# Optimization experiments

Hardware: AMD Instinct MI355X
Metric: run time of the kernel (lower is better)

The kernel has to match this reference:

```python
import jax, jax.numpy as jnp
import numpy as np

B, S, D, HEADS, E, HID = 4, 2048, 512, 8, 8, 1365  # HID = int(D*4*2/3) per Expert_alt
CF, THRESH, TOPN = 2.0, 0.2, 2                      # capacity_factor_eval, threshold_eval, top-2
BAL_COEF, Z_COEF = 0.01, 0.001


def setup_inputs():
    key = jax.random.key(0)
    ks = jax.random.split(key, 8)
    f32 = jnp.float32
    return {
        'x': jax.random.normal(ks[0], (B, S, D), f32),
        'Wqkv': jax.random.normal(ks[1], (3 * D, D), f32) * (D ** -0.5),
        'bqkv': jnp.zeros((3 * D,), f32),
        'Wo': jax.random.normal(ks[2], (D, D), f32) * (D ** -0.5),
        'bo': jnp.zeros((D,), f32),
        'Wg': jax.random.normal(ks[3], (D, E), f32) * (D ** -0.5),
        'ln_g': jnp.ones((E, D), f32),
        'ln_b': jnp.zeros((E, D), f32),
        'W1': jax.random.normal(ks[4], (E, D, HID), f32) * (D ** -0.5),
        'b1': jnp.zeros((E, HID), f32),
        'W2': jax.random.normal(ks[5], (E, HID, D), f32) * (HID ** -0.5),
        'b2': jnp.zeros((E, D), f32),
    }


def _moe(x, Wg, ln_g, ln_b, W1, b1, W2, b2):
    # top-2 gated MoE with capacity-factor dispatch, grouped expert FFN, combine
    Bq, Sq, Dq = x.shape
    Eq = Wg.shape[1]
    C = int(CF * Sq * TOPN / Eq)  # expert capacity per batch row
    logits = x @ Wg                              # [B,S,E]
    probs = jax.nn.softmax(logits, -1)
    gvals, gidx = jax.lax.top_k(probs, 2)        # [B,S,2]
    use2 = (gvals[..., 1] > THRESH).astype(x.dtype)
    # priority order: all top-1 assignments first, then top-2
    e_idx = jnp.concatenate([gidx[..., 0], gidx[..., 1]], axis=1)          # [B,2S]
    assigned = jnp.concatenate([jnp.ones((Bq, Sq), x.dtype), use2], axis=1)
    onehot = jax.nn.one_hot(e_idx, Eq, dtype=x.dtype) * assigned[..., None]
    pos = (jnp.cumsum(onehot, axis=1) * onehot).sum(-1) - 1.0              # slot within expert
    keep = ((assigned > 0) & (pos >= 0) & (pos < C)).astype(x.dtype)
    slot = jnp.where(keep > 0, pos, C).astype(jnp.int32)                   # overflow -> slot C (dropped)
    b_idx = jnp.broadcast_to(jnp.arange(Bq)[:, None], (Bq, 2 * Sq))
    x2 = jnp.concatenate([x, x], axis=1) * keep[..., None]
    disp = jnp.zeros((Bq, Eq, C + 1, Dq), x.dtype).at[b_idx, e_idx, slot].add(x2)
    # grouped expert FFN: LayerNorm -> Linear -> LeakyReLU -> Linear
    xe = disp[:, :, :C].transpose(1, 0, 2, 3).reshape(Eq, Bq * C, Dq)
    mu = xe.mean(-1, keepdims=True)
    var = xe.var(-1, keepdims=True)
    xn = (xe - mu) * jax.lax.rsqrt(var + 1e-5) * ln_g[:, None] + ln_b[:, None]
    h = jnp.einsum('etd,edh->eth', xn, W1) + b1[:, None]
    h = jnp.where(h > 0, h, 0.01 * h)  # LeakyReLU
    ye = jnp.einsum('eth,ehd->etd', h, W2) + b2[:, None]
    yb = ye.reshape(Eq, Bq, C, Dq).transpose(1, 0, 2, 3)                   # [B,E,C,D]
    yb = jnp.concatenate([yb, jnp.zeros((Bq, Eq, 1, Dq), x.dtype)], axis=2)
    y_tok = yb[b_idx, e_idx, slot]                                         # [B,2S,D]
    w = jnp.concatenate([gvals[..., 0], gvals[..., 1] * use2], axis=1) * keep
    out = (y_tok * w[..., None]).reshape(Bq, 2, Sq, Dq).sum(1)
    # aux losses
    top1 = jax.nn.one_hot(gidx[..., 0], Eq, dtype=x.dtype)
    density = top1.mean((0, 1))
    proxy = probs.mean((0, 1))
    balance = Eq * jnp.sum(density * proxy)
    zloss = jnp.mean(jax.nn.logsumexp(logits, -1) ** 2)
    total = BAL_COEF * balance + Z_COEF * zloss
    return out, total, balance, zloss


def reference(x, Wqkv, bqkv, Wo, bo, Wg, ln_g, ln_b, W1, b1, W2, b2):
    Bq, Sq, Dq = x.shape
    dh = Dq // HEADS
    qkv = x @ Wqkv.T + bqkv
    q, k, v = jnp.split(qkv, 3, -1)
    rs = lambda t: t.reshape(Bq, Sq, HEADS, dh).transpose(0, 2, 1, 3)
    q, k, v = rs(q), rs(k), rs(v)
    attn = jax.nn.softmax(jnp.einsum('bhqd,bhkd->bhqk', q, k) / np.float32(np.sqrt(dh)), -1)
    o = jnp.einsum('bhqk,bhkd->bhqd', attn, v).transpose(0, 2, 1, 3).reshape(Bq, Sq, Dq)
    o = o @ Wo.T + bo + x  # MHA + residual
    moe_out, total, bal, z = _moe(o, Wg, ln_g, ln_b, W1, b1, W2, b2)
    return moe_out + o, total, bal, z  # SparseMoEBlock residual; dropout is identity (eval)
```

## Files before the change

kernel.cpp:

```cpp
#include <hip/hip_runtime.h>
#include <hip/hip_bf16.h>
#include <math.h>

#define B_    4
#define S_    2048
#define D_    512
#define H_    8
#define DH_   64
#define E_    8
#define HID_  1365
#define HIDP_ 1408
#define CAP_  1024
#define TOK_  (B_*S_)
#define NASS_ (B_*2*S_)
#define RMAX_ (NASS_ + 8*128)
#define NQKU_ 1152
#define C11   (1.0f/2048.0f)
#define C22   (1.0f/(2048.0f*2048.0f))

typedef __attribute__((ext_vector_type(8))) short bf16x8;
typedef __attribute__((ext_vector_type(8))) _Float16 f16x8;
typedef __attribute__((ext_vector_type(4))) float f32x4;
typedef __hip_bfloat16 bf16;
typedef _Float16 f16;

#define MFMA16(a, b, c) __builtin_amdgcn_mfma_f32_16x16x32_bf16(a, b, c, 0, 0, 0)
#define MFMAH(a, b, c)  __builtin_amdgcn_mfma_f32_16x16x32_f16(a, b, c, 0, 0, 0)

__device__ __forceinline__ void gload16(const void* g, void* l) {
  __builtin_amdgcn_global_load_lds(
      (const __attribute__((address_space(1))) unsigned int*)g,
      (__attribute__((address_space(3))) unsigned int*)l, 16, 0, 0);
}

__device__ __forceinline__ unsigned bf16pk(float a, float b) {
  unsigned ua = __float_as_uint(a); ua = (ua + 0x7FFF + ((ua >> 16) & 1)) >> 16;
  unsigned ub = __float_as_uint(b); ub = (ub + 0x7FFF + ((ub >> 16) & 1)) >> 16;
  return ua | (ub << 16);
}

__device__ __forceinline__ unsigned short h2us(f16 h) {
  return *(unsigned short*)&h;
}

__global__ __launch_bounds__(256) void cvt_bf16(const float* __restrict__ in,
                                                bf16* __restrict__ out, int n) {
  int i = (blockIdx.x * 256 + threadIdx.x) * 4;
  if (i < n) {
    float4 v = *(const float4*)(in + i);
    uint2 pk; pk.x = bf16pk(v.x, v.y); pk.y = bf16pk(v.z, v.w);
    *(uint2*)((unsigned short*)out + i) = pk;
  }
}

__global__ __launch_bounds__(256) void cvt_f16(const float* __restrict__ in,
                                               f16* __restrict__ out, int n) {
  int i = (blockIdx.x * 256 + threadIdx.x) * 4;
  if (i < n) {
    float4 v = *(const float4*)(in + i);
    ushort4 o;
    ((unsigned short*)&o)[0] = h2us((f16)v.x);
    ((unsigned short*)&o)[1] = h2us((f16)v.y);
    ((unsigned short*)&o)[2] = h2us((f16)v.z);
    ((unsigned short*)&o)[3] = h2us((f16)v.w);
    *(ushort4*)((unsigned short*)out + i) = o;
  }
}

__global__ __launch_bounds__(256) void split2h(const float* __restrict__ in,
    unsigned short* __restrict__ ph, unsigned short* __restrict__ pl, int n) {
  int i = (blockIdx.x * 256 + threadIdx.x) * 4;
  if (i >= n) return;
  float4 v = *(const float4*)(in + i);
  float a[4] = {v.x, v.y, v.z, v.w};
  ushort4 hh, ll;
#pragma unroll
  for (int j = 0; j < 4; j++) {
    f16 h = (f16)a[j];
    float r = (a[j] - (float)h) * 2048.f;
    f16 l = (f16)r;
    ((unsigned short*)&hh)[j] = h2us(h);
    ((unsigned short*)&ll)[j] = h2us(l);
  }
  *(ushort4*)(ph + i) = hh;
  *(ushort4*)(pl + i) = ll;
}

__global__ __launch_bounds__(256) void transpose_w1(const float* __restrict__ W1,
                                                    bf16* __restrict__ W1t) {
  __shared__ float t[32][33];
  int e = blockIdx.z;
  int n0 = blockIdx.x * 32, d0 = blockIdx.y * 32;
  int tx = threadIdx.x & 31, ty = threadIdx.x >> 5;
  const float* in = W1 + (size_t)e * D_ * HID_;
  bf16* out = W1t + (size_t)e * HIDP_ * D_;
#pragma unroll
  for (int j = 0; j < 4; j++) {
    int d = d0 + ty + j * 8, n = n0 + tx;
    t[ty + j * 8][tx] = (n < HID_) ? in[(size_t)d * HID_ + n] : 0.f;
  }
  __syncthreads();
#pragma unroll
  for (int j = 0; j < 4; j++) {
    int n = n0 + ty + j * 8, d = d0 + tx;
    out[(size_t)n * D_ + d] = __float2bfloat16(t[tx][ty + j * 8]);
  }
}

__global__ __launch_bounds__(256) void transpose_w2(const float* __restrict__ W2,
                                                    bf16* __restrict__ W2t) {
  __shared__ float t[32][33];
  int e = blockIdx.z;
  int n0 = blockIdx.x * 32, k0 = blockIdx.y * 32;
  int tx = threadIdx.x & 31, ty = threadIdx.x >> 5;
  const float* in = W2 + (size_t)e * HID_ * D_;
  bf16* out = W2t + (size_t)e * D_ * HIDP_;
#pragma unroll
  for (int j = 0; j < 4; j++) {
    int k = k0 + ty + j * 8;
    t[ty + j * 8][tx] = (k < HID_) ? in[(size_t)k * D_ + n0 + tx] : 0.f;
  }
  __syncthreads();
#pragma unroll
  for (int j = 0; j < 4; j++) {
    int n = n0 + ty + j * 8, k = k0 + tx;
    out[(size_t)n * HIDP_ + k] = __float2bfloat16(t[tx][ty + j * 8]);
  }
}

__global__ __launch_bounds__(256) void transpose_v(const unsigned short* __restrict__ vbuf,
                                                   unsigned short* __restrict__ vT) {
  __shared__ unsigned short t[32][33];
  int bh = blockIdx.z;
  int b = bh >> 3, h = bh & 7;
  int s0 = blockIdx.x * 32, d0 = blockIdx.y * 32;
  int tx = threadIdx.x & 31, ty = threadIdx.x >> 5;
  const unsigned short* in = vbuf + (size_t)b * S_ * D_ + h * DH_;
#pragma unroll
  for (int j = 0; j < 4; j++)
    t[ty + j * 8][tx] = in[(size_t)(s0 + ty + j * 8) * D_ + d0 + tx];
  __syncthreads();
  unsigned short* out = vT + (size_t)bh * DH_ * S_;
#pragma unroll
  for (int j = 0; j < 4; j++)
    out[(size_t)(d0 + ty + j * 8) * S_ + s0 + tx] = t[tx][ty + j * 8];
}

__global__ __launch_bounds__(256) void transpose_u(const float* __restrict__ qku,
                                                   f16* __restrict__ U2T) {
  __shared__ float t[64][132];
  int b = blockIdx.y;
  int s0 = blockIdx.x * 64;
  int tid = threadIdx.x;
#pragma unroll
  for (int p = 0; p < 8; p++) {
    int i = tid + p * 256;
    int tok = i >> 5, c4 = i & 31;
    float4 v = *(const float4*)(qku + (size_t)(b * 2048 + s0 + tok) * NQKU_ + 1024 + c4 * 4);
    t[tok][c4 * 4 + 0] = v.x; t[tok][c4 * 4 + 1] = v.y;
    t[tok][c4 * 4 + 2] = v.z; t[tok][c4 * 4 + 3] = v.w;
  }
  __syncthreads();
  int row = tid >> 1, sh = tid & 1;
  int h = row >> 4, rr = row & 15;
  int e = rr & 7;
  bool lo = rr >= 8;
  f16* dst = U2T + ((size_t)((b * 8 + h) * 16 + rr) * 2048 + s0 + sh * 32);
  for (int i = 0; i < 32; i++) {
    float v = t[sh * 32 + i][h * 8 + e];
    f16 hh = (f16)v;
    f16 outv = lo ? (f16)((v - (float)hh) * 2048.f) : hh;
    dst[i] = outv;
  }
}

template <int MODE>
__global__ __launch_bounds__(256) void gemm_mfma(
    const bf16* __restrict__ A, const bf16* __restrict__ Bt,
    const float* __restrict__ bias, const float* __restrict__ resid,
    void* __restrict__ Cout, int N, int K,
    const int* __restrict__ ebase, const int* __restrict__ ecnt) {
  __shared__ bf16 Al[128 * 64];
  __shared__ bf16 Bl[128 * 64];
  int tid = threadIdx.x;
  int w = tid >> 6, lane = tid & 63;
  int lg = lane >> 4, li = lane & 15;
  int e = 0;
  size_t arow0;
  if constexpr (MODE >= 2) {
    e = blockIdx.z;
    int r0 = blockIdx.y * 128;
    if (r0 >= ecnt[e]) return;
    arow0 = (size_t)(ebase[e] + r0);
  } else {
    arow0 = (size_t)blockIdx.y * 128;
  }
  int n0 = blockIdx.x * 128;
  const bf16* Bexp = Bt + (size_t)e * N * K;

  int rowA[4], scA[4];
#pragma unroll
  for (int j = 0; j < 4; j++) {
    int o = w * 4096 + j * 1024 + lane * 16;
    rowA[j] = o >> 7;
    scA[j] = ((o >> 4) & 7) ^ (rowA[j] & 7);
  }
  int wm = w >> 1, wn = w & 1;
  f32x4 acc[4][4] = {};

  for (int k0 = 0; k0 < K; k0 += 64) {
#pragma unroll
    for (int j = 0; j < 4; j++) {
      int o = w * 4096 + j * 1024 + lane * 16;
      gload16(A + (arow0 + rowA[j]) * (size_t)K + k0 + scA[j] * 8, (char*)Al + o);
      gload16(Bexp + (size_t)(n0 + rowA[j]) * K + k0 + scA[j] * 8, (char*)Bl + o);
    }
    __syncthreads();
#pragma unroll
    for (int ks = 0; ks < 2; ks++) {
      bf16x8 af[4], bfr[4];
#pragma unroll
      for (int mi = 0; mi < 4; mi++) {
        int row = wm * 64 + mi * 16 + li;
        int cb = (lg * 16 + ks * 64) ^ ((row & 7) << 4);
        af[mi] = *(const bf16x8*)((char*)Al + row * 128 + cb);
      }
#pragma unroll
      for (int ni = 0; ni < 4; ni++) {
        int row = wn * 64 + ni * 16 + li;
        int cb = (lg * 16 + ks * 64) ^ ((row & 7) << 4);
        bfr[ni] = *(const bf16x8*)((char*)Bl + row * 128 + cb);
      }
#pragma unroll
      for (int mi = 0; mi < 4; mi++)
#pragma unroll
        for (int ni = 0; ni < 4; ni++)
          acc[mi][ni] = MFMA16(af[mi], bfr[ni], acc[mi][ni]);
    }
    __syncthreads();
  }

#pragma unroll
  for (int mi = 0; mi < 4; mi++) {
#pragma unroll
    for (int ni = 0; ni < 4; ni++) {
#pragma unroll
      for (int r = 0; r < 4; r++) {
        size_t m = arow0 + wm * 64 + mi * 16 + lg * 4 + r;
        int c = n0 + wn * 64 + ni * 16 + li;
        float v = acc[mi][ni][r];
        if constexpr (MODE == 1) {
          v += bias[c] + resid[m * (size_t)N + c];
          ((float*)Cout)[m * (size_t)N + c] = v;
        } else if constexpr (MODE == 2) {
          if (c < HID_) {
            v += bias[e * HID_ + c];
            v = (v > 0.f) ? v : 0.01f * v;
            ((bf16*)Cout)[m * (size_t)HIDP_ + c] = __float2bfloat16(v);
          } else {
            ((bf16*)Cout)[m * (size_t)HIDP_ + c] = __float2bfloat16(0.f);
          }
        } else {
          v += bias[e * D_ + c];
          ((bf16*)Cout)[m * (size_t)N + c] = __float2bfloat16(v);
        }
      }
    }
  }
}

__global__ __launch_bounds__(256) void gemm_vf16(
    const f16* __restrict__ A, const f16* __restrict__ Bt,
    const float* __restrict__ bias, f16* __restrict__ Cout, int N, int K) {
  __shared__ f16 Al[128 * 64];
  __shared__ f16 Bl[128 * 64];
  int tid = threadIdx.x;
  int w = tid >> 6, lane = tid & 63;
  int lg = lane >> 4, li = lane & 15;
  size_t arow0 = (size_t)blockIdx.y * 128;
  int n0 = blockIdx.x * 128;

  int rowA[4], scA[4];
#pragma unroll
  for (int j = 0; j < 4; j++) {
    int o = w * 4096 + j * 1024 + lane * 16;
    rowA[j] = o >> 7;
    scA[j] = ((o >> 4) & 7) ^ (rowA[j] & 7);
  }
  int wm = w >> 1, wn = w & 1;
  f32x4 acc[4][4] = {};

  for (int k0 = 0; k0 < K; k0 += 64) {
#pragma unroll
    for (int j = 0; j < 4; j++) {
      int o = w * 4096 + j * 1024 + lane * 16;
      gload16(A + (arow0 + rowA[j]) * (size_t)K + k0 + scA[j] * 8, (char*)Al + o);
      gload16(Bt + (size_t)(n0 + rowA[j]) * K + k0 + scA[j] * 8, (char*)Bl + o);
    }
    __syncthreads();
#pragma unroll
    for (int ks = 0; ks < 2; ks++) {
      f16x8 af[4], bfr[4];
#pragma unroll
      for (int mi = 0; mi < 4; mi++) {
        int row = wm * 64 + mi * 16 + li;
        int cb = (lg * 16 + ks * 64) ^ ((row & 7) << 4);
        af[mi] = *(const f16x8*)((char*)Al + row * 128 + cb);
      }
#pragma unroll
      for (int ni = 0; ni < 4; ni++) {
        int row = wn * 64 + ni * 16 + li;
        int cb = (lg * 16 + ks * 64) ^ ((row & 7) << 4);
        bfr[ni] = *(const f16x8*)((char*)Bl + row * 128 + cb);
      }
#pragma unroll
      for (int mi = 0; mi < 4; mi++)
#pragma unroll
        for (int ni = 0; ni < 4; ni++)
          acc[mi][ni] = MFMAH(af[mi], bfr[ni], acc[mi][ni]);
    }
    __syncthreads();
  }
#pragma unroll
  for (int mi = 0; mi < 4; mi++)
#pragma unroll
    for (int ni = 0; ni < 4; ni++)
#pragma unroll
      for (int r = 0; r < 4; r++) {
        size_t m = arow0 + wm * 64 + mi * 16 + lg * 4 + r;
        int c = n0 + wn * 64 + ni * 16 + li;
        Cout[m * (size_t)N + c] = (f16)(acc[mi][ni][r] + bias[c]);
      }
}

__global__ __launch_bounds__(256) void gemm_split2(
    const f16* __restrict__ Ah, const f16* __restrict__ Als,
    const f16* __restrict__ Bh, const f16* __restrict__ Bls,
    const float* __restrict__ bias, float* __restrict__ C, int N, int K) {
  __shared__ f16 Ls[4][128 * 32];
  const f16* Ap[2] = {Ah, Als};
  const f16* Bp[2] = {Bh, Bls};
  int tid = threadIdx.x;
  int w = tid >> 6, lane = tid & 63;
  int lg = lane >> 4, li = lane & 15;
  int lin = blockIdx.y * gridDim.x + blockIdx.x;
  int aa = lin / 72, t = lin % 72;
  size_t m0 = (size_t)((t & 7) + 8 * aa) * 128;
  int n0 = (t >> 3) * 128;
  int wm = w >> 1, wn = w & 1;
  f32x4 accA[4][4] = {};
  f32x4 accB[4][4] = {};

  for (int k0 = 0; k0 < K; k0 += 32) {
#pragma unroll
    for (int p = 0; p < 2; p++) {
#pragma unroll
      for (int j = 0; j < 2; j++) {
        int o = w * 2048 + j * 1024 + lane * 16;
        int row = o >> 6;
        int sc = ((o >> 4) & 3) ^ (row & 3);
        gload16(Ap[p] + (m0 + row) * (size_t)K + k0 + sc * 8, (char*)Ls[p] + o);
        gload16(Bp[p] + (size_t)(n0 + row) * K + k0 + sc * 8, (char*)Ls[2 + p] + o);
      }
    }
    __syncthreads();
    f16x8 afh[4], afl[4], bfh[4], bfl[4];
#pragma unroll
    for (int mi = 0; mi < 4; mi++) {
      int row = wm * 64 + mi * 16 + li;
      int cb = (lg * 16) ^ ((row & 3) << 4);
      afh[mi] = *(const f16x8*)((char*)Ls[0] + row * 64 + cb);
      afl[mi] = *(const f16x8*)((char*)Ls[1] + row * 64 + cb);
    }
#pragma unroll
    for (int ni = 0; ni < 4; ni++) {
      int row = wn * 64 + ni * 16 + li;
      int cb = (lg * 16) ^ ((row & 3) << 4);
      bfh[ni] = *(const f16x8*)((char*)Ls[2] + row * 64 + cb);
      bfl[ni] = *(const f16x8*)((char*)Ls[3] + row * 64 + cb);
    }
#pragma unroll
    for (int mi = 0; mi < 4; mi++)
#pragma unroll
      for (int ni = 0; ni < 4; ni++) {
        accA[mi][ni] = MFMAH(afh[mi], bfh[ni], accA[mi][ni]);
        accB[mi][ni] = MFMAH(afh[mi], bfl[ni], accB[mi][ni]);
        accB[mi][ni] = MFMAH(afl[mi], bfh[ni], accB[mi][ni]);
      }
    __syncthreads();
  }
#pragma unroll
  for (int mi = 0; mi < 4; mi++)
#pragma unroll
    for (int ni = 0; ni < 4; ni++)
#pragma unroll
      for (int r = 0; r < 4; r++) {
        size_t m = m0 + wm * 64 + mi * 16 + lg * 4 + r;
        int c = n0 + wn * 64 + ni * 16 + li;
        C[m * (size_t)N + c] = accA[mi][ni][r] + accB[mi][ni][r] * C11 + bias[c];
      }
}

__global__ __launch_bounds__(256) void ksplit(const float* __restrict__ qku,
    unsigned short* __restrict__ kh, unsigned short* __restrict__ kls) {
  int gid = blockIdx.x * 256 + threadIdx.x;
  int idx4 = gid * 4;
  int t = idx4 >> 9, c = idx4 & 511;
  int h = c >> 6, d = c & 63;
  int b = t >> 11, s = t & 2047;
  float4 v = *(const float4*)(qku + (size_t)t * NQKU_ + 512 + c);
  float a[4] = {v.x, v.y, v.z, v.w};
  ushort4 hh, ll;
#pragma unroll
  for (int j = 0; j < 4; j++) {
    f16 hv = (f16)a[j];
    f16 lv = (f16)((a[j] - (float)hv) * 2048.f);
    ((unsigned short*)&hh)[j] = h2us(hv);
    ((unsigned short*)&ll)[j] = h2us(lv);
  }
  size_t o = (((size_t)(b * 8 + h) * S_ + s) * 64 + d);
  *(ushort4*)(kh + o) = hh;
  *(ushort4*)(kls + o) = ll;
}

__global__ __launch_bounds__(256) void wg2_kernel(const float* __restrict__ Wo,
                                                  const float* __restrict__ Wg,
                                                  float* __restrict__ Wg2) {
  int gid = blockIdx.x * 256 + threadIdx.x;
  int d = gid >> 3, e = gid & 7;
  float acc = 0.f;
  for (int n = 0; n < D_; n++) acc += Wo[(size_t)n * D_ + d] * Wg[n * E_ + e];
  Wg2[d * E_ + e] = acc;
}

__global__ __launch_bounds__(256) void wu_kernel(const float* __restrict__ Wqkv,
    const float* __restrict__ Wg2, const float* __restrict__ bqkv,
    float* __restrict__ Wu, float* __restrict__ bfull) {
  int gid = blockIdx.x * 256 + threadIdx.x;
  int row = gid >> 9, d = gid & 511;
  float acc = 0.f;
  if (row < 64) {
    int h = row >> 3, e = row & 7;
    const float* wv = Wqkv + (size_t)(1024 + h * 64) * 512 + d;
    const float* wg = Wg2 + h * 64 * 8 + e;
    for (int c = 0; c < 64; c++) acc += wv[(size_t)c * 512] * wg[c * 8];
  }
  Wu[gid] = acc;
  if (gid < 1024) bfull[gid] = bqkv[gid];
  if (gid < 128) {
    float bacc = 0.f;
    if (gid < 64) {
      int h = gid >> 3, e = gid & 7;
      for (int c = 0; c < 64; c++)
        bacc += bqkv[1024 + h * 64 + c] * Wg2[(h * 64 + c) * 8 + e];
    }
    bfull[1024 + gid] = bacc;
  }
}

__global__ __launch_bounds__(256) void xwg_kernel(const float* __restrict__ x,
                                                  const float* __restrict__ bo,
                                                  const float* __restrict__ Wg,
                                                  float* __restrict__ logits) {
  int tid = threadIdx.x;
  int tl = tid >> 3, j = tid & 7;
  int t = blockIdx.x * 32 + tl;
  const float* xr = x + (size_t)t * D_;
  float part[8] = {0, 0, 0, 0, 0, 0, 0, 0};
  for (int d = j; d < D_; d += 8) {
    float xv = xr[d] + bo[d];
    const float* wg = Wg + d * E_;
#pragma unroll
    for (int e = 0; e < 8; e++) part[e] += xv * wg[e];
  }
#pragma unroll
  for (int off = 1; off < 8; off <<= 1)
#pragma unroll
    for (int e = 0; e < 8; e++) part[e] += __shfl_xor(part[e], off);
  if (j == 0) {
#pragma unroll
    for (int e = 0; e < 8; e++) logits[(size_t)t * 8 + e] = part[e];
  }
}

__global__ __launch_bounds__(512, 4) void attn_fused(
    const float* __restrict__ qku,
    const f16* __restrict__ kh, const f16* __restrict__ kls,
    const f16* __restrict__ vT, const f16* __restrict__ U2T,
    bf16* __restrict__ attnb, float* __restrict__ part) {
  __shared__ f16 Ks0[128 * 64];
  __shared__ f16 Ks1[128 * 64];
  __shared__ f16 Vtl[64 * 128];
  __shared__ f16 Ut[16 * 128];
  __shared__ f16 Pl[8][16 * 40];
  int bid = blockIdx.x;
  int xcd = bid & 7, idx = bid >> 3;
  int bh = (idx >> 4) * 8 + xcd;
  int qt = idx & 15;
  int b = bh >> 3, h = bh & 7, q0 = qt * 128;
  int tid = threadIdx.x, w = tid >> 6, lane = tid & 63;
  int lg = lane >> 4, qi = lane & 15;

  const float* qsrc = qku + (size_t)(b * S_ + q0 + w * 16 + qi) * NQKU_ + h * 64 + lg * 8;
  f16x8 qh[2], qls[2];
#pragma unroll
  for (int ks = 0; ks < 2; ks++) {
#pragma unroll
    for (int i = 0; i < 8; i++) {
      float xv = qsrc[ks * 32 + i];
      f16 hh = (f16)xv;
      f16 ll = (f16)((xv - (float)hh) * 2048.f);
      qh[ks][i] = hh;
      qls[ks][i] = ll;
    }
  }

  f32x4 oacc[4] = {};
  f32x4 raccA = {0.f, 0.f, 0.f, 0.f};
  f32x4 raccB = {0.f, 0.f, 0.f, 0.f};
  float mrun = -1e30f, lrun = 0.f;
  const f16* Vbase = vT + (size_t)bh * DH_ * S_;
  char* pw = (char*)&Pl[w][0];

  for (int kt = 0; kt < S_ / 128; kt++) {
#pragma unroll
    for (int j = 0; j < 2; j++) {
      int o = w * 2048 + j * 1024 + lane * 16;
      int row = o >> 7;
      int sc = ((o >> 4) & 7) ^ (row & 7);
      size_t srcK = ((size_t)bh * S_ + kt * 128 + row) * 64 + sc * 8;
      gload16(kh + srcK, (char*)Ks0 + o);
      gload16(kls + srcK, (char*)Ks1 + o);
      int rowv = o >> 8;
      int scv = ((o >> 4) & 15) ^ (rowv & 7);
      gload16(Vbase + (size_t)rowv * S_ + kt * 128 + scv * 8, (char*)Vtl + o);
    }
    if (w < 2) {
#pragma unroll
      for (int j = 0; j < 2; j++) {
        int o = w * 2048 + j * 1024 + lane * 16;
        int rowu = o >> 8;
        int scu = ((o >> 4) & 15) ^ (rowu & 7);
        gload16(U2T + ((size_t)(bh * 16 + rowu) * 2048 + kt * 128 + scu * 8),
                (char*)Ut + o);
      }
    }
    __syncthreads();

    f32x4 sA[8], sB[8];
#pragma unroll
    for (int nb = 0; nb < 8; nb++) {
      f32x4 z = {0.f, 0.f, 0.f, 0.f};
      sA[nb] = z; sB[nb] = z;
    }
#pragma unroll
    for (int ks = 0; ks < 2; ks++) {
#pragma unroll
      for (int nb = 0; nb < 8; nb++) {
        int row = nb * 16 + qi;
        int cb = (lg * 16 + ks * 64) ^ ((row & 7) << 4);
        f16x8 k0 = *(const f16x8*)((char*)Ks0 + row * 128 + cb);
        f16x8 k1 = *(const f16x8*)((char*)Ks1 + row * 128 + cb);
        sA[nb] = MFMAH(k0, qh[ks], sA[nb]);
        sB[nb] = MFMAH(k0, qls[ks], sB[nb]);
        sB[nb] = MFMAH(k1, qh[ks], sB[nb]);
      }
    }
    float tmax = -1e30f;
#pragma unroll
    for (int nb = 0; nb < 8; nb++)
#pragma unroll
      for (int r = 0; r < 4; r++) {
        float v = (sA[nb][r] + sB[nb][r] * C11) * 0.125f;
        sA[nb][r] = v;
        tmax = fmaxf(tmax, v);
      }
    tmax = fmaxf(tmax, __shfl_xor(tmax, 16));
    tmax = fmaxf(tmax, __shfl_xor(tmax, 32));
    float mnew = fmaxf(mrun, tmax);
    float fsc = __expf(mrun - mnew);
    float psum = 0.f;
#pragma unroll
    for (int nb = 0; nb < 8; nb++)
#pragma unroll
      for (int r = 0; r < 4; r++) {
        float pv = __expf(sA[nb][r] - mnew);
        sA[nb][r] = pv;
        psum += pv;
      }
    psum += __shfl_xor(psum, 16);
    psum += __shfl_xor(psum, 32);
    lrun = lrun * fsc + psum;
    mrun = mnew;
#pragma unroll
    for (int r = 0; r < 4; r++) { raccA[r] *= fsc; raccB[r] *= fsc; }
#pragma unroll
    for (int db = 0; db < 4; db++)
#pragma unroll
      for (int r = 0; r < 4; r++) oacc[db][r] *= fsc;

#pragma unroll
    for (int c = 0; c < 4; c++) {
      float pv[8]; f16 phv[8];
#pragma unroll
      for (int nbL = 0; nbL < 2; nbL++)
#pragma unroll
        for (int rp = 0; rp < 2; rp++) {
          int nb = c * 2 + nbL;
          float p0 = sA[nb][rp * 2], p1 = sA[nb][rp * 2 + 1];
          f16 h0 = (f16)p0, h1 = (f16)p1;
          int ii = (nbL * 2 + rp) * 2;
          pv[ii] = p0; pv[ii + 1] = p1; phv[ii] = h0; phv[ii + 1] = h1;
          unsigned wd = (unsigned)h2us(h0) | ((unsigned)h2us(h1) << 16);
          int keyl = 4 * lg + 2 * rp + 16 * nbL;
          *(unsigned*)(pw + qi * 80 + keyl * 2) = wd;
        }
      f16x8 pf = *(const f16x8*)(pw + qi * 80 + lg * 16);
#pragma unroll
      for (int db = 0; db < 4; db++) {
        int row = db * 16 + qi;
        int cb = (lg * 16 + c * 64) ^ ((row & 7) << 4);
        f16x8 vf = *(const f16x8*)((char*)Vtl + row * 256 + cb);
        oacc[db] = MFMAH(vf, pf, oacc[db]);
      }
      int ua = qi * 256 + ((c * 64 + lg * 16) ^ ((qi & 7) << 4));
      f16x8 uf = *(const f16x8*)((char*)Ut + ua);
      raccA = MFMAH(uf, pf, raccA);
#pragma unroll
      for (int nbL = 0; nbL < 2; nbL++)
#pragma unroll
        for (int rp = 0; rp < 2; rp++) {
          int ii = (nbL * 2 + rp) * 2;
          f16 l0 = (f16)((pv[ii] - (float)phv[ii]) * 2048.f);
          f16 l1 = (f16)((pv[ii + 1] - (float)phv[ii + 1]) * 2048.f);
          unsigned wd = (unsigned)h2us(l0) | ((unsigned)h2us(l1) << 16);
          int keyl = 4 * lg + 2 * rp + 16 * nbL;
          *(unsigned*)(pw + qi * 80 + keyl * 2) = wd;
        }
      f16x8 pfl = *(const f16x8*)(pw + qi * 80 + lg * 16);
      raccB = MFMAH(uf, pfl, raccB);
    }
    __syncthreads();
  }

  float inv = 1.f / lrun;
  f32x4 pA, pB;
#pragma unroll
  for (int r = 0; r < 4; r++) {
    pA[r] = __shfl_xor(raccA[r], 32);
    pB[r] = __shfl_xor(raccB[r], 32);
  }
  if (lg < 2) {
    float* dst = part + ((size_t)bh * S_ + q0 + w * 16 + qi) * 8 + lg * 4;
#pragma unroll
    for (int r = 0; r < 4; r++)
      dst[r] = (raccA[r] + C11 * (pA[r] + raccB[r]) + C22 * pB[r]) * inv;
  }
  char* ow = (char*)Ks0 + w * 2048;
#pragma unroll
  for (int db = 0; db < 4; db++)
#pragma unroll
    for (int rp = 0; rp < 2; rp++) {
      int d = db * 16 + lg * 4 + rp * 2;
      unsigned pk = bf16pk(oacc[db][rp * 2] * inv, oacc[db][rp * 2 + 1] * inv);
      int addr = (qi * 128 + d * 2) ^ ((qi & 7) << 4);
      *(unsigned*)(ow + addr) = pk;
    }
#pragma unroll
  for (int j = 0; j < 2; j++) {
    int o = j * 1024 + lane * 16;
    int q = o >> 7;
    int c16 = (o >> 4) & 7;
    int sc = c16 ^ (q & 7);
    bf16x8 vv = *(const bf16x8*)(ow + q * 128 + sc * 16);
    *(bf16x8*)(attnb + ((size_t)(b * S_ + q0 + w * 16 + q)) * D_ + h * DH_ + c16 * 8) = vv;
  }
}

__global__ __launch_bounds__(256) void reduce_gate(
    const float* __restrict__ xwg, const float* __restrict__ part,
    int* __restrict__ e1a, int* __restrict__ e2a,
    float* __restrict__ g1a, float* __restrict__ g2a, int* __restrict__ use2a,
    float* __restrict__ dacc) {
  int t = blockIdx.x * 256 + threadIdx.x;
  int b = t >> 11, s = t & 2047;
  float lg[8];
#pragma unroll
  for (int e = 0; e < 8; e++) lg[e] = xwg[(size_t)t * 8 + e];
  for (int h = 0; h < 8; h++) {
    const float* pp = part + ((size_t)(b * 8 + h) * S_ + s) * 8;
#pragma unroll
    for (int e = 0; e < 8; e++) lg[e] += pp[e];
  }
  float mx = lg[0];
#pragma unroll
  for (int e = 1; e < 8; e++) mx = fmaxf(mx, lg[e]);
  float p[8], se = 0.f;
#pragma unroll
  for (int e = 0; e < 8; e++) { p[e] = expf(lg[e] - mx); se += p[e]; }
  float inv = 1.f / se;
#pragma unroll
  for (int e = 0; e < 8; e++) p[e] *= inv;
  float lse = logf(se) + mx;
  int a1 = 0; float m1 = p[0];
#pragma unroll
  for (int e = 1; e < 8; e++) if (p[e] > m1) { m1 = p[e]; a1 = e; }
  int a2 = -1; float m2 = -1.f;
#pragma unroll
  for (int e = 0; e < 8; e++) if (e != a1 && p[e] > m2) { m2 = p[e]; a2 = e; }
  e1a[t] = a1; e2a[t] = a2; g1a[t] = m1; g2a[t] = m2;
  use2a[t] = (m2 > 0.2f) ? 1 : 0;
  float z = lse * lse;
  float pr[8];
#pragma unroll
  for (int e = 0; e < 8; e++) pr[e] = p[e];
#pragma unroll
  for (int off = 1; off < 64; off <<= 1) {
#pragma unroll
    for (int e = 0; e < 8; e++) pr[e] += __shfl_xor(pr[e], off);
    z += __shfl_xor(z, off);
  }
  float dcnt[8];
#pragma unroll
  for (int e = 0; e < 8; e++) dcnt[e] = (float)__popcll(__ballot(a1 == e));
  if ((threadIdx.x & 63) == 0) {
#pragma unroll
    for (int e = 0; e < 8; e++) {
      atomicAdd(&dacc[e], dcnt[e]);
      atomicAdd(&dacc[8 + e], pr[e]);
    }
    atomicAdd(&dacc[16], z);
  }
}

__global__ __launch_bounds__(512) void scan_kernel(
    const int* __restrict__ e1a, const int* __restrict__ e2a,
    const int* __restrict__ use2a,
    int* __restrict__ posArr, int* __restrict__ kept_be) {
  __shared__ int wcnt[8][8];
  int b = blockIdx.x;
  int w = threadIdx.x >> 6, lane = threadIdx.x & 63;
  unsigned long long below = (1ull << lane) - 1ull;
  int cnt[8] = {0, 0, 0, 0, 0, 0, 0, 0};
  int ev[8], av[8];
#pragma unroll
  for (int it = 0; it < 8; it++) {
    int i = w * 512 + it * 64 + lane;
    int s = i & (S_ - 1);
    int t = b * S_ + s;
    int e, a;
    if (i < S_) { e = e1a[t]; a = 1; }
    else        { e = e2a[t]; a = use2a[t]; }
    ev[it] = e; av[it] = a;
#pragma unroll
    for (int ee = 0; ee < 8; ee++)
      cnt[ee] += __popcll(__ballot(a && (e == ee)));
  }
  if (lane == 0)
#pragma unroll
    for (int ee = 0; ee < 8; ee++) wcnt[w][ee] = cnt[ee];
  __syncthreads();
  int run[8];
#pragma unroll
  for (int ee = 0; ee < 8; ee++) {
    int sB = 0;
    for (int ww = 0; ww < w; ww++) sB += wcnt[ww][ee];
    run[ee] = sB;
  }
#pragma unroll
  for (int it = 0; it < 8; it++) {
    int i = w * 512 + it * 64 + lane;
    int e = ev[it], a = av[it];
    int pos = -1;
#pragma unroll
    for (int ee = 0; ee < 8; ee++) {
      unsigned long long mask = __ballot(a && (e == ee));
      if (a && e == ee) pos = run[ee] + __popcll(mask & below);
      run[ee] += __popcll(mask);
    }
    posArr[b * (2 * S_) + i] = (a && pos < CAP_) ? pos : -1;
  }
  if (w == 7 && lane == 0)
#pragma unroll
    for (int ee = 0; ee < 8; ee++) kept_be[b * 8 + ee] = min(run[ee], CAP_);
}

__global__ void finalize_meta(const int* __restrict__ kept_be,
                              int* __restrict__ ebase, int* __restrict__ bbase,
                              int* __restrict__ ecnt,
                              const float* __restrict__ dacc, float* __restrict__ outs) {
  if (threadIdx.x == 0 && blockIdx.x == 0) {
    int base = 0;
    for (int e = 0; e < 8; e++) {
      int tot = 0;
      for (int b = 0; b < 4; b++) { bbase[b * 8 + e] = tot; tot += kept_be[b * 8 + e]; }
      ecnt[e] = tot;
      ebase[e] = base;
      base += (tot + 127) & ~127;
    }
    float bal = 0.f;
    for (int e = 0; e < 8; e++) bal += (dacc[e] / (float)TOK_) * (dacc[8 + e] / (float)TOK_);
    bal *= (float)E_;
    float z = dacc[16] / (float)TOK_;
    outs[0] = 0.01f * bal + 0.001f * z;
    outs[1] = bal;
    outs[2] = z;
  }
}

__global__ __launch_bounds__(256) void scatter_kernel(
    const int* __restrict__ posArr, const int* __restrict__ e1a, const int* __restrict__ e2a,
    const float* __restrict__ g1a, const float* __restrict__ g2a,
    const int* __restrict__ ebase, const int* __restrict__ bbase,
    int* __restrict__ rowtok, int* __restrict__ rowexp,
    int* __restrict__ tokidx, float* __restrict__ tokw) {
  int gi = blockIdx.x * 256 + threadIdx.x;
  int b = gi >> 12, i = gi & 4095;
  int k = i >> 11, s = i & (S_ - 1);
  int t = b * S_ + s;
  int pos = posArr[gi];
  int idx = -1; float w = 0.f;
  if (pos >= 0) {
    int e = k ? e2a[t] : e1a[t];
    idx = ebase[e] + bbase[b * 8 + e] + pos;
    rowtok[idx] = t;
    rowexp[idx] = e;
    w = k ? g2a[t] : g1a[t];
  }
  tokidx[k * TOK_ + t] = idx;
  tokw[k * TOK_ + t] = w;
}

__global__ __launch_bounds__(256) void ln_kernel(
    const float* __restrict__ o2, const int* __restrict__ rowtok,
    const int* __restrict__ rowexp, const float* __restrict__ ln_g,
    const float* __restrict__ ln_b, bf16* __restrict__ xn) {
  int row = blockIdx.x * 4 + (threadIdx.x >> 6);
  int lane = threadIdx.x & 63;
  int tok = rowtok[row];
  if (tok < 0) return;
  int e = rowexp[row];
  const float* xr = o2 + (size_t)tok * D_;
  float v[8], sum = 0.f, sq = 0.f;
#pragma unroll
  for (int j = 0; j < 8; j++) { v[j] = xr[lane * 8 + j]; sum += v[j]; sq += v[j] * v[j]; }
#pragma unroll
  for (int off = 1; off < 64; off <<= 1) { sum += __shfl_xor(sum, off); sq += __shfl_xor(sq, off); }
  float mu = sum / (float)D_;
  float var = sq / (float)D_ - mu * mu;
  float inv = rsqrtf(var + 1e-5f);
  bf16* xo = xn + (size_t)row * D_;
#pragma unroll
  for (int j = 0; j < 8; j++) {
    int d = lane * 8 + j;
    xo[d] = __float2bfloat16((v[j] - mu) * inv * ln_g[e * D_ + d] + ln_b[e * D_ + d]);
  }
}

__global__ __launch_bounds__(256) void combine_kernel(
    const float* __restrict__ o2, const bf16* __restrict__ y,
    const int* __restrict__ tokidx, const float* __restrict__ tokw,
    float* __restrict__ out) {
  size_t gi = (size_t)blockIdx.x * 256 + threadIdx.x;
  int t = (int)(gi >> 9);
  int d = (int)(gi & (D_ - 1));
  float v = o2[gi];
  int i1 = tokidx[t], i2 = tokidx[TOK_ + t];
  if (i1 >= 0) v += tokw[t] * __bfloat162float(y[(size_t)i1 * D_ + d]);
  if (i2 >= 0) v += tokw[TOK_ + t] * __bfloat162float(y[(size_t)i2 * D_ + d]);
  out[gi] = v;
}

extern "C" void kernel_launch(void* const* d_in, const int* in_sizes, int n_in,
                              void* d_out, int out_size, void* d_ws, size_t ws_size,
                              hipStream_t stream) {
  const float* x    = (const float*)d_in[0];
  const float* Wqkv = (const float*)d_in[1];
  const float* bqkv = (const float*)d_in[2];
  const float* Wo   = (const float*)d_in[3];
  const float* bo   = (const float*)d_in[4];
  const float* Wg   = (const float*)d_in[5];
  const float* ln_g = (const float*)d_in[6];
  const float* ln_b = (const float*)d_in[7];
  const float* W1   = (const float*)d_in[8];
  const float* b1   = (const float*)d_in[9];
  const float* W2   = (const float*)d_in[10];
  const float* b2   = (const float*)d_in[11];
  float* out = (float*)d_out;

  char* ws = (char*)d_ws;
  size_t off = 0;
  auto alloc = [&](size_t bytes) -> void* {
    void* p = ws + off;
    off = (off + bytes + 255) & ~(size_t)255;
    return p;
  };
  float* qku32 = (float*)alloc((size_t)TOK_ * NQKU_ * 4);
  f16*  vbuf   = (f16*)alloc((size_t)TOK_ * D_ * 2);
  f16*  vT     = (f16*)alloc((size_t)B_ * H_ * DH_ * S_ * 2);
  bf16* attnb  = (bf16*)alloc((size_t)TOK_ * D_ * 2);
  float* o2    = (float*)alloc((size_t)TOK_ * D_ * 4);
  f16*  xh     = (f16*)alloc((size_t)TOK_ * D_ * 2);
  f16*  xls    = (f16*)alloc((size_t)TOK_ * D_ * 2);
  f16*  Wqh    = (f16*)alloc((size_t)NQKU_ * D_ * 2);
  f16*  Wqls   = (f16*)alloc((size_t)NQKU_ * D_ * 2);
  f16*  Wvh    = (f16*)alloc((size_t)D_ * D_ * 2);
  bf16* Wob    = (bf16*)alloc((size_t)D_ * D_ * 2);
  bf16* W1t    = (bf16*)alloc((size_t)E_ * HIDP_ * D_ * 2);
  bf16* W2t    = (bf16*)alloc((size_t)E_ * D_ * HIDP_ * 2);
  bf16* xn     = (bf16*)alloc((size_t)RMAX_ * D_ * 2);
  bf16* hbuf   = (bf16*)alloc((size_t)RMAX_ * HIDP_ * 2);
  bf16* ybuf   = (bf16*)alloc((size_t)RMAX_ * D_ * 2);
  float* Wg2   = (float*)alloc(D_ * E_ * 4);
  float* Wu    = (float*)alloc((size_t)128 * D_ * 4);
  float* bfull = (float*)alloc(NQKU_ * 4);
  f16*  U2T    = (f16*)alloc((size_t)32 * 16 * 2048 * 2);
  float* logits= (float*)alloc((size_t)TOK_ * 8 * 4);
  float* part  = (float*)alloc((size_t)B_ * H_ * S_ * 8 * 4);
  int*   e1a   = (int*)alloc(TOK_ * 4);
  int*   e2a   = (int*)alloc(TOK_ * 4);
  int*   use2a = (int*)alloc(TOK_ * 4);
  float* g1a   = (float*)alloc(TOK_ * 4);
  float* g2a   = (float*)alloc(TOK_ * 4);
  int*   posArr  = (int*)alloc(NASS_ * 4);
  int*   kept_be = (int*)alloc(32 * 4);
  int*   ebase   = (int*)alloc(8 * 4);
  int*   bbase   = (int*)alloc(32 * 4);
  int*   ecnt    = (int*)alloc(8 * 4);
  int*   rowtok  = (int*)alloc(RMAX_ * 4);
  int*   rowexp  = (int*)alloc(RMAX_ * 4);
  int*   tokidx  = (int*)alloc(NASS_ * 4);
  float* tokw    = (float*)alloc(NASS_ * 4);
  float* dacc    = (float*)alloc(32 * 4);
  f16* kh  = xh;
  f16* kls = xls;

  hipMemsetAsync(dacc, 0, 32 * 4, stream);
  hipMemsetAsync(rowtok, 0xFF, RMAX_ * 4, stream);

  split2h<<<TOK_ * D_ / 4 / 256, 256, 0, stream>>>(x, (unsigned short*)xh,
                                                   (unsigned short*)xls, TOK_ * D_);
  split2h<<<1024 * D_ / 4 / 256, 256, 0, stream>>>(Wqkv, (unsigned short*)Wqh,
                                                   (unsigned short*)Wqls, 1024 * D_);
  cvt_f16<<<D_ * D_ / 4 / 256, 256, 0, stream>>>(Wqkv + (size_t)1024 * D_, Wvh, D_ * D_);
  cvt_bf16<<<D_ * D_ / 4 / 256, 256, 0, stream>>>(Wo, Wob, D_ * D_);
  transpose_w1<<<dim3(44, 16, 8), 256, 0, stream>>>(W1, W1t);
  transpose_w2<<<dim3(16, 44, 8), 256, 0, stream>>>(W2, W2t);
  wg2_kernel<<<16, 256, 0, stream>>>(Wo, Wg, Wg2);
  wu_kernel<<<256, 256, 0, stream>>>(Wqkv, Wg2, bqkv, Wu, bfull);
  split2h<<<128 * D_ / 4 / 256, 256, 0, stream>>>(Wu,
      (unsigned short*)(Wqh + (size_t)1024 * D_),
      (unsigned short*)(Wqls + (size_t)1024 * D_), 128 * D_);

  gemm_split2<<<dim3(9, 64), 256, 0, stream>>>(xh, xls, Wqh, Wqls,
                                               bfull, qku32, NQKU_, D_);
  gemm_vf16<<<dim3(4, 64), 256, 0, stream>>>(xh, Wvh, bqkv + 1024, vbuf, D_, D_);
  ksplit<<<TOK_ * 512 / 4 / 256, 256, 0, stream>>>(qku32, (unsigned short*)kh,
                                                   (unsigned short*)kls);
  transpose_u<<<dim3(32, 4), 256, 0, stream>>>(qku32, U2T);
  xwg_kernel<<<TOK_ / 32, 256, 0, stream>>>(x, bo, Wg, logits);
  transpose_v<<<dim3(64, 2, 32), 256, 0, stream>>>((const unsigned short*)vbuf,
                                                   (unsigned short*)vT);

  attn_fused<<<dim3(512), 512, 0, stream>>>(qku32, kh, kls, vT, U2T,
                                            attnb, part);
  gemm_mfma<1><<<dim3(4, 64), 256, 0, stream>>>(attnb, Wob, bo, x, o2,
                                                D_, D_, nullptr, nullptr);
  reduce_gate<<<TOK_ / 256, 256, 0, stream>>>(logits, part, e1a, e2a, g1a, g2a,
                                              use2a, dacc);
  scan_kernel<<<B_, 512, 0, stream>>>(e1a, e2a, use2a, posArr, kept_be);
  finalize_meta<<<1, 64, 0, stream>>>(kept_be, ebase, bbase, ecnt, dacc,
                                      out + (size_t)TOK_ * D_);
  scatter_kernel<<<NASS_ / 256, 256, 0, stream>>>(posArr, e1a, e2a, g1a, g2a,
                                                  ebase, bbase, rowtok, rowexp,
                                                  tokidx, tokw);
  ln_kernel<<<RMAX_ / 4, 256, 0, stream>>>(o2, rowtok, rowexp, ln_g, ln_b, xn);
  gemm_mfma<2><<<dim3(HIDP_ / 128, 32, E_), 256, 0, stream>>>(xn, W1t, b1, nullptr, hbuf,
                                                              HIDP_, D_, ebase, ecnt);
  gemm_mfma<3><<<dim3(D_ / 128, 32, E_), 256, 0, stream>>>(hbuf, W2t, b2, nullptr, ybuf,
                                                           D_, HIDP_, ebase, ecnt);
  combine_kernel<<<(TOK_ * D_) / 256, 256, 0, stream>>>(o2, ybuf, tokidx, tokw, out);
}
```

Before: 500.7 us.

## Widen split-GEMM K tile and streamline attention softmax with lazy rescale

The split-precision GEMM now stages a K-tile of 64 instead of 32 with 8-way XOR swizzle, halving barrier count per K and precomputing load offsets. The attention kernel folds the scale and log2e into a single FMA and switches to exp2f. It skips the running-max rescale unless the tile max exceeds the current max by more than 8, and packs the hi/lo f16 splits with cvt_pkrtz into separate LDS buffers so the lo pass no longer overwrites the hi buffer. Risks include more LDS per GEMM block, which may lower occupancy, round-toward-zero conversion, and values up to 2^8 in the deferred-rescale path.

```diff
diff --git a/kernel.cpp b/kernel.cpp
--- a/kernel.cpp
+++ b/kernel.cpp
@@ -20,6 +20,7 @@
 
 typedef __attribute__((ext_vector_type(8))) short bf16x8;
 typedef __attribute__((ext_vector_type(8))) _Float16 f16x8;
+typedef __attribute__((ext_vector_type(2))) __fp16 h16x2;
 typedef __attribute__((ext_vector_type(4))) float f32x4;
 typedef __hip_bfloat16 bf16;
 typedef _Float16 f16;
@@ -337,9 +338,8 @@
     const f16* __restrict__ Ah, const f16* __restrict__ Als,
     const f16* __restrict__ Bh, const f16* __restrict__ Bls,
     const float* __restrict__ bias, float* __restrict__ C, int N, int K) {
-  __shared__ f16 Ls[4][128 * 32];
-  const f16* Ap[2] = {Ah, Als};
-  const f16* Bp[2] = {Bh, Bls};
+  __shared__ f16 As[2][128 * 64];
+  __shared__ f16 Bs[2][128 * 64];
   int tid = threadIdx.x;
   int w = tid >> 6, lane = tid & 63;
   int lg = lane >> 4, li = lane & 15;
@@ -351,42 +351,52 @@
   f32x4 accA[4][4] = {};
   f32x4 accB[4][4] = {};
 
-  for (int k0 = 0; k0 < K; k0 += 32) {
-#pragma unroll
-    for (int p = 0; p < 2; p++) {
-#pragma unroll
-      for (int j = 0; j < 2; j++) {
-        int o = w * 2048 + j * 1024 + lane * 16;
-        int row = o >> 6;
-        int sc = ((o >> 4) & 3) ^ (row & 3);
-        gload16(Ap[p] + (m0 + row) * (size_t)K + k0 + sc * 8, (char*)Ls[p] + o);
-        gload16(Bp[p] + (size_t)(n0 + row) * K + k0 + sc * 8, (char*)Ls[2 + p] + o);
-      }
+  int rowA[4], scA[4];
+#pragma unroll
+  for (int j = 0; j < 4; j++) {
+    int o = w * 4096 + j * 1024 + lane * 16;
+    rowA[j] = o >> 7;
+    scA[j] = ((o >> 4) & 7) ^ (rowA[j] & 7);
+  }
+
+  for (int k0 = 0; k0 < K; k0 += 64) {
+#pragma unroll
+    for (int j = 0; j < 4; j++) {
+      int o = w * 4096 + j * 1024 + lane * 16;
+      size_t sa = (m0 + rowA[j]) * (size_t)K + k0 + scA[j] * 8;
+      size_t sb = ((size_t)n0 + rowA[j]) * K + k0 + scA[j] * 8;
+      gload16(Ah + sa, (char*)As[0] + o);
+      gload16(Als + sa, (char*)As[1] + o);
+      gload16(Bh + sb, (char*)Bs[0] + o);
+      gload16(Bls + sb, (char*)Bs[1] + o);
     }
     __syncthreads();
-    f16x8 afh[4], afl[4], bfh[4], bfl[4];
-#pragma unroll
-    for (int mi = 0; mi < 4; mi++) {
-      int row = wm * 64 + mi * 16 + li;
-      int cb = (lg * 16) ^ ((row & 3) << 4);
-      afh[mi] = *(const f16x8*)((char*)Ls[0] + row * 64 + cb);
-      afl[mi] = *(const f16x8*)((char*)Ls[1] + row * 64 + cb);
-    }
-#pragma unroll
-    for (int ni = 0; ni < 4; ni++) {
-      int row = wn * 64 + ni * 16 + li;
-      int cb = (lg * 16) ^ ((row & 3) << 4);
-      bfh[ni] = *(const f16x8*)((char*)Ls[2] + row * 64 + cb);
-      bfl[ni] = *(const f16x8*)((char*)Ls[3] + row * 64 + cb);
-    }
-#pragma unroll
-    for (int mi = 0; mi < 4; mi++)
+#pragma unroll
+    for (int ks = 0; ks < 2; ks++) {
+      f16x8 afh[4], afl[4], bfh[4], bfl[4];
+#pragma unroll
+      for (int mi = 0; mi < 4; mi++) {
+        int row = wm * 64 + mi * 16 + li;
+        int cb = (lg * 16 + ks * 64) ^ ((row & 7) << 4);
+        afh[mi] = *(const f16x8*)((char*)As[0] + row * 128 + cb);
+        afl[mi] = *(const f16x8*)((char*)As[1] + row * 128 + cb);
+      }
 #pragma unroll
       for (int ni = 0; ni < 4; ni++) {
-        accA[mi][ni] = MFMAH(afh[mi], bfh[ni], accA[mi][ni]);
-        accB[mi][ni] = MFMAH(afh[mi], bfl[ni], accB[mi][ni]);
-        accB[mi][ni] = MFMAH(afl[mi], bfh[ni], accB[mi][ni]);
-      }
+        int row = wn * 64 + ni * 16 + li;
+        int cb = (lg * 16 + ks * 64) ^ ((row & 7) << 4);
+        bfh[ni] = *(const f16x8*)((char*)Bs[0] + row * 128 + cb);
+        bfl[ni] = *(const f16x8*)((char*)Bs[1] + row * 128 + cb);
+      }
+#pragma unroll
+      for (int mi = 0; mi < 4; mi++)
+#pragma unroll
+        for (int ni = 0; ni < 4; ni++) {
+          accA[mi][ni] = MFMAH(afh[mi], bfh[ni], accA[mi][ni]);
+          accB[mi][ni] = MFMAH(afh[mi], bfl[ni], accB[mi][ni]);
+          accB[mi][ni] = MFMAH(afl[mi], bfh[ni], accB[mi][ni]);
+        }
+    }
     __syncthreads();
   }
 #pragma unroll
@@ -492,7 +502,8 @@
   __shared__ f16 Ks1[128 * 64];
   __shared__ f16 Vtl[64 * 128];
   __shared__ f16 Ut[16 * 128];
-  __shared__ f16 Pl[8][16 * 40];
+  __shared__ f16 PlH[8][16 * 40];
+  __shared__ f16 PlL[8][16 * 40];
   int bid = blockIdx.x;
   int xcd = bid & 7, idx = bid >> 3;
   int bh = (idx >> 4) * 8 + xcd;
@@ -500,6 +511,8 @@
   int b = bh >> 3, h = bh & 7, q0 = qt * 128;
   int tid = threadIdx.x, w = tid >> 6, lane = tid & 63;
   int lg = lane >> 4, qi = lane & 15;
+  const float KS = 0.125f * 1.44269504089f;
+  const float KS2 = KS * C11;
 
   const float* qsrc = qku + (size_t)(b * S_ + q0 + w * 16 + qi) * NQKU_ + h * 64 + lg * 8;
   f16x8 qh[2], qls[2];
@@ -520,7 +533,8 @@
   f32x4 raccB = {0.f, 0.f, 0.f, 0.f};
   float mrun = -1e30f, lrun = 0.f;
   const f16* Vbase = vT + (size_t)bh * DH_ * S_;
-  char* pw = (char*)&Pl[w][0];
+  char* pwh = (char*)&PlH[w][0];
+  char* pwl = (char*)&PlL[w][0];
 
   for (int kt = 0; kt < S_ / 128; kt++) {
 #pragma unroll
@@ -571,51 +585,61 @@
     for (int nb = 0; nb < 8; nb++)
 #pragma unroll
       for (int r = 0; r < 4; r++) {
-        float v = (sA[nb][r] + sB[nb][r] * C11) * 0.125f;
+        float v = sA[nb][r] * KS + sB[nb][r] * KS2;
         sA[nb][r] = v;
         tmax = fmaxf(tmax, v);
       }
     tmax = fmaxf(tmax, __shfl_xor(tmax, 16));
     tmax = fmaxf(tmax, __shfl_xor(tmax, 32));
-    float mnew = fmaxf(mrun, tmax);
-    float fsc = __expf(mrun - mnew);
+    float fsc = 1.f;
+    if (!__all(tmax <= mrun + 8.f)) {
+      float mnew = fmaxf(mrun, tmax);
+      fsc = exp2f(mrun - mnew);
+      mrun = mnew;
+#pragma unroll
+      for (int r = 0; r < 4; r++) { raccA[r] *= fsc; raccB[r] *= fsc; }
+#pragma unroll
+      for (int db = 0; db < 4; db++)
+#pragma unroll
+        for (int r = 0; r < 4; r++) oacc[db][r] *= fsc;
+    }
     float psum = 0.f;
 #pragma unroll
     for (int nb = 0; nb < 8; nb++)
 #pragma unroll
       for (int r = 0; r < 4; r++) {
-        float pv = __expf(sA[nb][r] - mnew);
+        float pv = exp2f(sA[nb][r] - mrun);
         sA[nb][r] = pv;
         psum += pv;
       }
     psum += __shfl_xor(psum, 16);
     psum += __shfl_xor(psum, 32);
     lrun = lrun * fsc + psum;
-    mrun = mnew;
-#pragma unroll
-    for (int r = 0; r < 4; r++) { raccA[r] *= fsc; raccB[r] *= fsc; }
-#pragma unroll
-    for (int db = 0; db < 4; db++)
-#pragma unroll
-      for (int r = 0; r < 4; r++) oacc[db][r] *= fsc;
+
+    unsigned hwv[16], lwv[16];
+#pragma unroll
+    for (int nb = 0; nb < 8; nb++)
+#pragma unroll
+      for (int rp = 0; rp < 2; rp++) {
+        float p0 = sA[nb][rp * 2], p1 = sA[nb][rp * 2 + 1];
+        h16x2 hp = __builtin_amdgcn_cvt_pkrtz(p0, p1);
+        float b0 = (float)hp[0], b1 = (float)hp[1];
+        h16x2 lp = __builtin_amdgcn_cvt_pkrtz((p0 - b0) * 2048.f, (p1 - b1) * 2048.f);
+        hwv[nb * 2 + rp] = *(unsigned*)&hp;
+        lwv[nb * 2 + rp] = *(unsigned*)&lp;
+      }
 
 #pragma unroll
     for (int c = 0; c < 4; c++) {
-      float pv[8]; f16 phv[8];
 #pragma unroll
       for (int nbL = 0; nbL < 2; nbL++)
 #pragma unroll
         for (int rp = 0; rp < 2; rp++) {
-          int nb = c * 2 + nbL;
-          float p0 = sA[nb][rp * 2], p1 = sA[nb][rp * 2 + 1];
-          f16 h0 = (f16)p0, h1 = (f16)p1;
-          int ii = (nbL * 2 + rp) * 2;
-          pv[ii] = p0; pv[ii + 1] = p1; phv[ii] = h0; phv[ii + 1] = h1;
-          unsigned wd = (unsigned)h2us(h0) | ((unsigned)h2us(h1) << 16);
           int keyl = 4 * lg + 2 * rp + 16 * nbL;
-          *(unsigned*)(pw + qi * 80 + keyl * 2) = wd;
+          *(unsigned*)(pwh + qi * 80 + keyl * 2) = hwv[(c * 2 + nbL) * 2 + rp];
+          *(unsigned*)(pwl + qi * 80 + keyl * 2) = lwv[(c * 2 + nbL) * 2 + rp];
         }
-      f16x8 pf = *(const f16x8*)(pw + qi * 80 + lg * 16);
+      f16x8 pf = *(const f16x8*)(pwh + qi * 80 + lg * 16);
 #pragma unroll
       for (int db = 0; db < 4; db++) {
         int row = db * 16 + qi;
@@ -626,18 +650,7 @@
       int ua = qi * 256 + ((c * 64 + lg * 16) ^ ((qi & 7) << 4));
       f16x8 uf = *(const f16x8*)((char*)Ut + ua);
       raccA = MFMAH(uf, pf, raccA);
-#pragma unroll
-      for (int nbL = 0; nbL < 2; nbL++)
-#pragma unroll
-        for (int rp = 0; rp < 2; rp++) {
-          int ii = (nbL * 2 + rp) * 2;
-          f16 l0 = (f16)((pv[ii] - (float)phv[ii]) * 2048.f);
-          f16 l1 = (f16)((pv[ii + 1] - (float)phv[ii + 1]) * 2048.f);
-          unsigned wd = (unsigned)h2us(l0) | ((unsigned)h2us(l1) << 16);
-          int keyl = 4 * lg + 2 * rp + 16 * nbL;
-          *(unsigned*)(pw + qi * 80 + keyl * 2) = wd;
-        }
-      f16x8 pfl = *(const f16x8*)(pw + qi * 80 + lg * 16);
+      f16x8 pfl = *(const f16x8*)(pwl + qi * 80 + lg * 16);
       raccB = MFMAH(uf, pfl, raccB);
     }
     __syncthreads();
```

New measurement: 509.4 us. Within noise of the previous version (+1.7%).
